# Performance work log

Hardware: AMD Instinct MI355X
Metric: run time of the kernel (lower is better)

Reference implementation:

```python
import jax, jax.numpy as jnp
import numpy as np

TOPK = 9
NUM_CLASSES = 80
EPS = 1e-9
IMG = 1280
STRIDES = (8, 16, 32)


def _make_anchors():
    boxes = []
    for s in STRIDES:
        n = IMG // s
        c = (np.arange(n, dtype=np.float32) + 0.5) * s
        cy, cx = np.meshgrid(c, c, indexing='ij')
        cx = cx.reshape(-1); cy = cy.reshape(-1)
        half = s * 2.5
        boxes.append(np.stack([cx - half, cy - half, cx + half, cy + half], axis=-1))
    return jnp.asarray(np.concatenate(boxes, axis=0), jnp.float32)


def setup_inputs() -> dict:
    key = jax.random.key(0)
    k1, k2, k3 = jax.random.split(key, 3)
    B, M = 16, 64
    xy = jax.random.uniform(k1, (B, M, 2), jnp.float32, 0.0, 1100.0)
    wh = jax.random.uniform(k2, (B, M, 2), jnp.float32, 8.0, 180.0)
    gt_bboxes = jnp.concatenate([xy, xy + wh], axis=-1)
    gt_labels = jax.random.randint(k3, (B, M, 1), 0, NUM_CLASSES, jnp.int32)
    pad_gt_mask = (jnp.arange(M) < 56).astype(jnp.float32)[None, :, None] * jnp.ones((B, 1, 1), jnp.float32)
    return {
        'anchor_bboxes': _make_anchors(),
        'num_anchors_list': [25600, 6400, 1600],
        'gt_labels': gt_labels,
        'gt_bboxes': gt_bboxes,
        'pad_gt_mask': pad_gt_mask,
        'bg_index': NUM_CLASSES,
    }


def _atss(anchor_bboxes, num_anchors_list, gt_labels, gt_bboxes, pad_gt_mask, bg_index):
    B, M, _ = gt_bboxes.shape
    A = anchor_bboxes.shape[0]
    f32 = gt_bboxes.dtype

    # pairwise IoU [B, M, A]
    area_g = (gt_bboxes[..., 2] - gt_bboxes[..., 0]) * (gt_bboxes[..., 3] - gt_bboxes[..., 1])
    area_a = (anchor_bboxes[:, 2] - anchor_bboxes[:, 0]) * (anchor_bboxes[:, 3] - anchor_bboxes[:, 1])
    lt = jnp.maximum(gt_bboxes[..., None, :2], anchor_bboxes[None, None, :, :2])
    rb = jnp.minimum(gt_bboxes[..., None, 2:], anchor_bboxes[None, None, :, 2:])
    wh = jnp.clip(rb - lt, 0.0)
    overlap = wh[..., 0] * wh[..., 1]
    ious = overlap / (area_g[..., None] + area_a[None, None, :] - overlap + EPS)

    # center distances [B, M, A]
    gt_c = (gt_bboxes[..., :2] + gt_bboxes[..., 2:]) * 0.5
    an_c = (anchor_bboxes[:, :2] + anchor_bboxes[:, 2:]) * 0.5
    dist = jnp.linalg.norm(gt_c[:, :, None, :] - an_c[None, None, :, :], axis=-1)

    # per-pyramid-level topk (smallest distance)
    valid = pad_gt_mask > 0  # [B, M, 1]
    row = jnp.arange(B * M)[:, None]
    is_in_topk_parts, topk_idx_parts = [], []
    start = 0
    for n in num_anchors_list:
        d = dist[..., start:start + n]
        _, idxs = jax.lax.top_k(-d, TOPK)  # [B, M, TOPK]
        topk_idx_parts.append(idxs + start)
        idxs_m = jnp.where(valid, idxs, 0)
        counts = jnp.zeros((B * M, n), jnp.int32).at[row, idxs_m.reshape(B * M, TOPK)].add(1)
        counts = counts.reshape(B, M, n)
        is_in = jnp.where(counts > 1, 0, counts).astype(f32)  # zero duplicates (padded gts)
        is_in_topk_parts.append(is_in)
        start += n
    is_in_topk = jnp.concatenate(is_in_topk_parts, axis=-1)  # [B, M, A]
    topk_idxs = jnp.concatenate(topk_idx_parts, axis=-1)     # [B, M, TOPK * n_levels]

    # adaptive IoU threshold per gt: mean + std of candidate ious
    iou_candidates = ious * is_in_topk
    cand = jnp.take_along_axis(iou_candidates, topk_idxs, axis=-1)
    thr = cand.mean(axis=-1, keepdims=True) + jnp.std(cand, axis=-1, ddof=1, keepdims=True)
    is_in_topk = jnp.where(iou_candidates > thr, is_in_topk, jnp.zeros_like(is_in_topk))

    # anchor centers inside gt boxes [B, M, A]
    cx, cy = an_c[:, 0], an_c[:, 1]
    l = cx[None, None, :] - gt_bboxes[..., 0:1]
    t = cy[None, None, :] - gt_bboxes[..., 1:2]
    r = gt_bboxes[..., 2:3] - cx[None, None, :]
    b = gt_bboxes[..., 3:4] - cy[None, None, :]
    is_in_gts = (jnp.minimum(jnp.minimum(l, t), jnp.minimum(r, b)) > EPS).astype(f32)

    mask_positive = is_in_topk * is_in_gts * pad_gt_mask
    mps = mask_positive.sum(axis=-2)  # [B, A]

    # resolve anchors assigned to multiple gts via max-iou gt
    argm = ious.argmax(axis=-2)  # [B, A]
    is_max_iou = (jnp.arange(M)[None, :, None] == argm[:, None, :]).astype(f32)
    mask_multi = (mps[:, None, :] > 1)
    mask_positive = jnp.where(mask_multi, is_max_iou, mask_positive)
    mps = mask_positive.sum(axis=-2)

    assigned_gt_index = mask_positive.argmax(axis=-2)  # [B, A]
    assigned_labels = jnp.take_along_axis(gt_labels[..., 0], assigned_gt_index, axis=1)
    assigned_labels = jnp.where(mps > 0, assigned_labels, jnp.full_like(assigned_labels, bg_index))
    assigned_bboxes = jnp.take_along_axis(gt_bboxes, assigned_gt_index[..., None], axis=1)  # [B, A, 4]
    assigned_scores = jax.nn.one_hot(assigned_labels, NUM_CLASSES + 1, dtype=jnp.float32)[..., :NUM_CLASSES]
    return assigned_labels.astype(jnp.int32), assigned_bboxes, assigned_scores


def reference(anchor_bboxes, num_anchors_list, gt_labels, gt_bboxes, pad_gt_mask, bg_index):
    return _atss(anchor_bboxes, list(num_anchors_list), gt_labels, gt_bboxes, pad_gt_mask, bg_index)
```

## Files before the change

kernel.cpp:

```cpp
#include <hip/hip_runtime.h>
#include <stdint.h>


constexpr int A_TOT = 33600;
constexpr int NB    = 16;
constexpr int NM    = 64;
constexpr int NCLS  = 80;
constexpr int NBA   = NB * A_TOT;

__device__ __forceinline__ void anchor_geom(int a, float& cx, float& cy,
                                            float& half, float& area) {
    if (a < 25600) {
        int row = a / 160, col = a - row * 160;
        cx = (col + 0.5f) * 8.0f;  cy = (row + 0.5f) * 8.0f;
        half = 20.0f; area = 1600.0f;
    } else if (a < 32000) {
        int j = a - 25600; int row = j / 80, col = j - row * 80;
        cx = (col + 0.5f) * 16.0f; cy = (row + 0.5f) * 16.0f;
        half = 40.0f; area = 6400.0f;
    } else {
        int j = a - 32000; int row = j / 40, col = j - row * 40;
        cx = (col + 0.5f) * 32.0f; cy = (row + 0.5f) * 32.0f;
        half = 80.0f; area = 25600.0f;
    }
}

__device__ __forceinline__ float iou_box(float gx1, float gy1, float gx2, float gy2,
                                         float areag, float cx, float cy,
                                         float half, float areaa) {
    float ax1 = cx - half, ay1 = cy - half, ax2 = cx + half, ay2 = cy + half;
    float ltx = fmaxf(gx1, ax1), lty = fmaxf(gy1, ay1);
    float rbx = fminf(gx2, ax2), rby = fminf(gy2, ay2);
    float w = fmaxf(rbx - ltx, 0.0f), h = fmaxf(rby - lty, 0.0f);
    float ov = w * h;
    return ov / (areag + areaa - ov + 1e-9f);
}

template <int START, int N1, int S>
__device__ __forceinline__ void window_level(int lane, float gcx, float gcy,
                                             uint64_t* cand_out ) {
    float tx = gcx / (float)S - 0.5f;
    float ty = gcy / (float)S - 0.5f;
    int c0 = (int)floorf(tx) - 6; c0 = min(max(c0, 0), N1 - 13);
    int r0 = (int)floorf(ty) - 6; r0 = min(max(r0, 0), N1 - 13);

    uint64_t k9[9];
#pragma unroll
    for (int i = 0; i < 9; ++i) k9[i] = ~0ull;

    for (int k = lane; k < 169; k += 64) {
        int wr = k / 13, wc = k - wr * 13;
        int row = r0 + wr, col = c0 + wc;
        float cx = (col + 0.5f) * (float)S;
        float cy = (row + 0.5f) * (float)S;
        float dx = gcx - cx, dy = gcy - cy;
        float d  = sqrtf(dx * dx + dy * dy);
        uint64_t key = ((uint64_t)__float_as_uint(d) << 32)
                     | (uint32_t)(START + row * N1 + col);
        if (key < k9[8]) {
            uint64_t x = key;
#pragma unroll
            for (int i = 0; i < 9; ++i) {
                if (x < k9[i]) { uint64_t t = k9[i]; k9[i] = x; x = t; }
            }
        }
    }

    for (int r = 0; r < 9; ++r) {
        unsigned long long v = (unsigned long long)k9[0];
#pragma unroll
        for (int off = 1; off < 64; off <<= 1) {
            unsigned long long o = __shfl_xor(v, off, 64);
            if (o < v) v = o;
        }
        if ((uint64_t)v == k9[0]) {
#pragma unroll
            for (int i = 0; i < 8; ++i) k9[i] = k9[i + 1];
            k9[8] = ~0ull;
        }
        if (lane == 0) cand_out[r] = (uint64_t)v;
    }
}

__global__ __launch_bounds__(64) void atss_topk(
    const float* __restrict__ gt_bboxes,
    const float* __restrict__ pad_mask,
    uint32_t* __restrict__ packed)
{
    int bm = blockIdx.x;
    if (pad_mask[bm] <= 0.0f) return;
    int b = bm >> 6, m = bm & 63;
    int lane = threadIdx.x;

    float4 g = ((const float4*)gt_bboxes)[bm];
    float gcx = (g.x + g.z) * 0.5f, gcy = (g.y + g.w) * 0.5f;
    float areag = (g.z - g.x) * (g.w - g.y);

    __shared__ uint64_t cand[27];
    __shared__ float    iou_s[27];
    __shared__ int      ok_s[27];

    window_level<0,     160,  8>(lane, gcx, gcy, cand + 0);
    window_level<25600,  80, 16>(lane, gcx, gcy, cand + 9);
    window_level<32000,  40, 32>(lane, gcx, gcy, cand + 18);
    __syncthreads();

    int aidx = 0; float iou = 0.0f;
    if (lane < 27) {
        aidx = (int)(cand[lane] & 0xffffffffu);
        float cx, cy, half, areaa;
        anchor_geom(aidx, cx, cy, half, areaa);
        iou = iou_box(g.x, g.y, g.z, g.w, areag, cx, cy, half, areaa);
        float l = cx - g.x, t = cy - g.y, r = g.z - cx, btm = g.w - cy;
        float mn = fminf(fminf(l, t), fminf(r, btm));
        iou_s[lane] = iou;
        ok_s[lane]  = (mn > 1e-9f) ? 1 : 0;
    }
    __syncthreads();

    float sum = 0.0f;
#pragma unroll
    for (int i = 0; i < 27; ++i) sum += iou_s[i];
    float mean = sum / 27.0f;
    float var = 0.0f;
#pragma unroll
    for (int i = 0; i < 27; ++i) { float d = iou_s[i] - mean; var += d * d; }
    float thr = mean + sqrtf(var / 26.0f);

    if (lane < 27 && ok_s[lane] && iou > thr) {
        atomicAdd(&packed[b * A_TOT + aidx], (1u << 20) | (uint32_t)m);
    }
}

__global__ __launch_bounds__(256) void atss_finalize(
    const float* __restrict__ gt_bboxes,
    const int*   __restrict__ gt_labels,
    const uint32_t* __restrict__ packed,
    float* __restrict__ out)
{
    int tid = blockIdx.x * 256 + threadIdx.x;
    int b = tid / A_TOT;
    int a = tid - b * A_TOT;

    uint32_t pk = packed[tid];
    int c = (int)(pk >> 20);
    int gidx = 0;
    if (c == 1) {
        gidx = (int)(pk & 0xfffffu);
    } else if (c > 1) {
        float cx, cy, half, areaa;
        anchor_geom(a, cx, cy, half, areaa);
        const float4* gb = (const float4*)(gt_bboxes) + b * NM;
        float best = -1.0f; int bi = 0;
        for (int mm = 0; mm < NM; ++mm) {
            float4 g = gb[mm];
            float areag = (g.z - g.x) * (g.w - g.y);
            float iou = iou_box(g.x, g.y, g.z, g.w, areag, cx, cy, half, areaa);
            if (iou > best) { best = iou; bi = mm; }
        }
        gidx = bi;
    }

    int label = (c > 0) ? gt_labels[b * NM + gidx] : NCLS;
    out[tid] = (float)label;
    float4 gsel = ((const float4*)gt_bboxes)[b * NM + gidx];
    ((float4*)(out + NBA))[tid] = gsel;

    __shared__ int lab_s[256];
    lab_s[threadIdx.x] = label;
    __syncthreads();

    float4* sc4 = (float4*)(out + (size_t)NBA * 5)
                + (size_t)blockIdx.x * (256 * 20);
#pragma unroll
    for (int i = 0; i < 20; ++i) {
        int k  = threadIdx.x + i * 256;
        int al = k / 20;
        int c4 = k - al * 20;
        int lab = lab_s[al];
        int base = c4 * 4;
        float4 v;
        v.x = (base + 0 == lab) ? 1.0f : 0.0f;
        v.y = (base + 1 == lab) ? 1.0f : 0.0f;
        v.z = (base + 2 == lab) ? 1.0f : 0.0f;
        v.w = (base + 3 == lab) ? 1.0f : 0.0f;
        sc4[k] = v;
    }
}

__global__ void atss_init(uint32_t* __restrict__ packed) {
    int i = blockIdx.x * 256 + threadIdx.x;
    if (i < NBA) packed[i] = 0u;
}

extern "C" void kernel_launch(void* const* d_in, const int* in_sizes, int n_in,
                              void* d_out, int out_size, void* d_ws, size_t ws_size,
                              hipStream_t stream) {
    const int*   gt_labels = (const int*)d_in[2];
    const float* gt_bboxes = (const float*)d_in[3];
    const float* pad_mask  = (const float*)d_in[4];
    float* out = (float*)d_out;

    uint32_t* packed = (uint32_t*)d_ws;

    atss_init<<<(NBA + 255) / 256, 256, 0, stream>>>(packed);

    atss_topk<<<NB * NM, 64, 0, stream>>>(gt_bboxes, pad_mask, packed);

    atss_finalize<<<NBA / 256, 256, 0, stream>>>(
        gt_bboxes, gt_labels, packed, out);
}
```

Baseline: 209.3 us.

## Split finalize into assign and scores kernels with nontemporal stores

Splits the finalize kernel into two. The first computes labels and boxes and writes an int label array to workspace. The second expands labels into the one-hot score tensor with nontemporal vector stores over more, smaller blocks. The goal is better write throughput for the large score output and more parallelism for that write. The cost is an extra kernel launch and an extra round trip of the labels through global memory.

```diff
diff --git a/kernel.cpp b/kernel.cpp
--- a/kernel.cpp
+++ b/kernel.cpp
@@ -7,6 +7,8 @@
 constexpr int NM    = 64;
 constexpr int NCLS  = 80;
 constexpr int NBA   = NB * A_TOT;
+
+typedef float vfloat4 __attribute__((ext_vector_type(4)));
 
 __device__ __forceinline__ void anchor_geom(int a, float& cx, float& cy,
                                             float& half, float& area) {
@@ -132,11 +134,12 @@
     }
 }
 
-__global__ __launch_bounds__(256) void atss_finalize(
+__global__ __launch_bounds__(256) void atss_assign(
     const float* __restrict__ gt_bboxes,
     const int*   __restrict__ gt_labels,
     const uint32_t* __restrict__ packed,
-    float* __restrict__ out)
+    float* __restrict__ out,
+    int*   __restrict__ labels_i)
 {
     int tid = blockIdx.x * 256 + threadIdx.x;
     int b = tid / A_TOT;
@@ -162,29 +165,32 @@
     }
 
     int label = (c > 0) ? gt_labels[b * NM + gidx] : NCLS;
-    out[tid] = (float)label;
-    float4 gsel = ((const float4*)gt_bboxes)[b * NM + gidx];
-    ((float4*)(out + NBA))[tid] = gsel;
-
-    __shared__ int lab_s[256];
-    lab_s[threadIdx.x] = label;
-    __syncthreads();
-
-    float4* sc4 = (float4*)(out + (size_t)NBA * 5)
-                + (size_t)blockIdx.x * (256 * 20);
-#pragma unroll
-    for (int i = 0; i < 20; ++i) {
-        int k  = threadIdx.x + i * 256;
+    labels_i[tid] = label;
+    __builtin_nontemporal_store((float)label, out + tid);
+    const vfloat4* gb4 = (const vfloat4*)gt_bboxes;
+    vfloat4 gsel = gb4[b * NM + gidx];
+    __builtin_nontemporal_store(gsel, (vfloat4*)(out + NBA) + tid);
+}
+
+__global__ __launch_bounds__(256) void atss_scores(
+    const int* __restrict__ labels_i,
+    float* __restrict__ scores)
+{
+    vfloat4* s4 = (vfloat4*)scores;
+    int k0 = blockIdx.x * 2048 + threadIdx.x;
+#pragma unroll
+    for (int i = 0; i < 8; ++i) {
+        int k  = k0 + i * 256;
         int al = k / 20;
         int c4 = k - al * 20;
-        int lab = lab_s[al];
+        int lab = labels_i[al];
         int base = c4 * 4;
-        float4 v;
+        vfloat4 v;
         v.x = (base + 0 == lab) ? 1.0f : 0.0f;
         v.y = (base + 1 == lab) ? 1.0f : 0.0f;
         v.z = (base + 2 == lab) ? 1.0f : 0.0f;
         v.w = (base + 3 == lab) ? 1.0f : 0.0f;
-        sc4[k] = v;
+        __builtin_nontemporal_store(v, s4 + k);
     }
 }
 
@@ -201,12 +207,16 @@
     const float* pad_mask  = (const float*)d_in[4];
     float* out = (float*)d_out;
 
-    uint32_t* packed = (uint32_t*)d_ws;
+    uint32_t* packed   = (uint32_t*)d_ws;
+    int*      labels_i = (int*)d_ws + NBA;
 
     atss_init<<<(NBA + 255) / 256, 256, 0, stream>>>(packed);
 
     atss_topk<<<NB * NM, 64, 0, stream>>>(gt_bboxes, pad_mask, packed);
 
-    atss_finalize<<<NBA / 256, 256, 0, stream>>>(
-        gt_bboxes, gt_labels, packed, out);
-}
+    atss_assign<<<NBA / 256, 256, 0, stream>>>(
+        gt_bboxes, gt_labels, packed, out, labels_i);
+
+    atss_scores<<<(NBA * 20) / 2048, 256, 0, stream>>>(
+        labels_i, out + (size_t)NBA * 5);
+}
```

Result: slower. 221.5 us (+5.8%).

## Shrink top-k window to 6x6 with rank-based selection; memset workspace

Applied to the files above, without the earlier changes.

The per-level nearest-anchor search window shrinks from 13x13 to 6x6. Selection changes from a per-lane insertion sort plus nine wave-wide shuffle reductions to a direct rank count in shared memory, where each of 36 lanes counts smaller keys and writes itself if its rank is below nine. The custom zero-init kernel is replaced with hipMemsetAsync. The smaller window cuts latency in the topk kernel, but it relies on a 6x6 neighbourhood always holding the nine nearest anchors, which is tight near clamped borders.

```diff
diff --git a/kernel.cpp b/kernel.cpp
--- a/kernel.cpp
+++ b/kernel.cpp
@@ -37,49 +37,36 @@
 }
 
 template <int START, int N1, int S>
-__device__ __forceinline__ void window_level(int lane, float gcx, float gcy,
-                                             uint64_t* cand_out ) {
+__device__ __forceinline__ void window_rank(int lane, float gcx, float gcy,
+                                            uint64_t* keys36,
+                                            uint64_t* cand_out ) {
     float tx = gcx / (float)S - 0.5f;
     float ty = gcy / (float)S - 0.5f;
-    int c0 = (int)floorf(tx) - 6; c0 = min(max(c0, 0), N1 - 13);
-    int r0 = (int)floorf(ty) - 6; r0 = min(max(r0, 0), N1 - 13);
+    int c0 = (int)floorf(tx) - 2; c0 = min(max(c0, 0), N1 - 6);
+    int r0 = (int)floorf(ty) - 2; r0 = min(max(r0, 0), N1 - 6);
 
-    uint64_t k9[9];
-#pragma unroll
-    for (int i = 0; i < 9; ++i) k9[i] = ~0ull;
-
-    for (int k = lane; k < 169; k += 64) {
-        int wr = k / 13, wc = k - wr * 13;
+    uint64_t mykey = ~0ull;
+    if (lane < 36) {
+        int wr = lane / 6, wc = lane - wr * 6;
         int row = r0 + wr, col = c0 + wc;
         float cx = (col + 0.5f) * (float)S;
         float cy = (row + 0.5f) * (float)S;
         float dx = gcx - cx, dy = gcy - cy;
         float d  = sqrtf(dx * dx + dy * dy);
-        uint64_t key = ((uint64_t)__float_as_uint(d) << 32)
-                     | (uint32_t)(START + row * N1 + col);
-        if (key < k9[8]) {
-            uint64_t x = key;
+        mykey = ((uint64_t)__float_as_uint(d) << 32)
+              | (uint32_t)(START + row * N1 + col);
+        keys36[lane] = mykey;
+    }
+    __syncthreads();
+
+    if (lane < 36) {
+        int rank = 0;
 #pragma unroll
-            for (int i = 0; i < 9; ++i) {
-                if (x < k9[i]) { uint64_t t = k9[i]; k9[i] = x; x = t; }
-            }
-        }
+        for (int j = 0; j < 36; ++j)
+            rank += (keys36[j] < mykey) ? 1 : 0;
+        if (rank < 9) cand_out[rank] = mykey;
     }
-
-    for (int r = 0; r < 9; ++r) {
-        unsigned long long v = (unsigned long long)k9[0];
-#pragma unroll
-        for (int off = 1; off < 64; off <<= 1) {
-            unsigned long long o = __shfl_xor(v, off, 64);
-            if (o < v) v = o;
-        }
-        if ((uint64_t)v == k9[0]) {
-#pragma unroll
-            for (int i = 0; i < 8; ++i) k9[i] = k9[i + 1];
-            k9[8] = ~0ull;
-        }
-        if (lane == 0) cand_out[r] = (uint64_t)v;
-    }
+    __syncthreads();
 }
 
 __global__ __launch_bounds__(64) void atss_topk(
@@ -96,14 +83,14 @@
     float gcx = (g.x + g.z) * 0.5f, gcy = (g.y + g.w) * 0.5f;
     float areag = (g.z - g.x) * (g.w - g.y);
 
+    __shared__ uint64_t keys36[36];
     __shared__ uint64_t cand[27];
     __shared__ float    iou_s[27];
     __shared__ int      ok_s[27];
 
-    window_level<0,     160,  8>(lane, gcx, gcy, cand + 0);
-    window_level<25600,  80, 16>(lane, gcx, gcy, cand + 9);
-    window_level<32000,  40, 32>(lane, gcx, gcy, cand + 18);
-    __syncthreads();
+    window_rank<0,     160,  8>(lane, gcx, gcy, keys36, cand + 0);
+    window_rank<25600,  80, 16>(lane, gcx, gcy, keys36, cand + 9);
+    window_rank<32000,  40, 32>(lane, gcx, gcy, keys36, cand + 18);
 
     int aidx = 0; float iou = 0.0f;
     if (lane < 27) {
@@ -188,11 +175,6 @@
     }
 }
 
-__global__ void atss_init(uint32_t* __restrict__ packed) {
-    int i = blockIdx.x * 256 + threadIdx.x;
-    if (i < NBA) packed[i] = 0u;
-}
-
 extern "C" void kernel_launch(void* const* d_in, const int* in_sizes, int n_in,
                               void* d_out, int out_size, void* d_ws, size_t ws_size,
                               hipStream_t stream) {
@@ -203,7 +185,7 @@
 
     uint32_t* packed = (uint32_t*)d_ws;
 
-    atss_init<<<(NBA + 255) / 256, 256, 0, stream>>>(packed);
+    hipMemsetAsync(packed, 0, (size_t)NBA * sizeof(uint32_t), stream);
 
     atss_topk<<<NB * NM, 64, 0, stream>>>(gt_bboxes, pad_mask, packed);
 
```

Measured after the change: 198.5 us. -5.2%, faster.
